# Kernel tuning notes

Measured on AMD Instinct MI355X. Metric: run time of the kernel, lower is better.

Reference implementation:

```python
import jax, jax.numpy as jnp
import numpy as np

N, D, H, E, K = 8192, 1024, 2048, 8, 2
LN_EPS = 1e-5


def setup_inputs() -> dict:
    key = jax.random.key(0)
    ks = jax.random.split(key, 9)
    s_in = 1.0 / np.sqrt(D)
    s_h = 1.0 / np.sqrt(H)
    return {
        "x": jax.random.normal(ks[0], (N, D), jnp.float32),
        "W1": jax.random.uniform(ks[1], (E, D, H), jnp.float32, -s_in, s_in),
        "b1": jax.random.uniform(ks[2], (E, H), jnp.float32, -s_in, s_in),
        "ln_g": jnp.ones((E, H), jnp.float32),
        "ln_b": jnp.zeros((E, H), jnp.float32),
        "W2": jax.random.uniform(ks[3], (E, H, H), jnp.float32, -s_h, s_h),
        "b2": jax.random.uniform(ks[4], (E, H), jnp.float32, -s_h, s_h),
        "Wg": jax.random.uniform(ks[5], (D, E), jnp.float32, -s_in, s_in),
        "bg": jax.random.uniform(ks[6], (E,), jnp.float32, -s_in, s_in),
    }


def _moe(x, W1, b1, ln_g, ln_b, W2, b2, Wg, bg):
    # Gate: softmax over experts, then top-k and renormalize
    gate = jax.nn.softmax(x @ Wg + bg, axis=-1)          # [N, E]
    top_w, top_i = jax.lax.top_k(gate, K)                 # [N, K]
    top_w = top_w / jnp.sum(top_w, axis=-1, keepdims=True)

    # Dense all-expert FFN (faithful to the original: compute every expert)
    h = jnp.einsum('nd,edh->neh', x, W1) + b1[None]       # [N, E, H]
    mu = jnp.mean(h, axis=-1, keepdims=True)
    var = jnp.mean(jnp.square(h - mu), axis=-1, keepdims=True)
    h = (h - mu) * jax.lax.rsqrt(var + LN_EPS) * ln_g[None] + ln_b[None]
    h = jax.nn.gelu(h, approximate=False)                 # torch GELU default = erf
    eo = jnp.einsum('neh,ehk->nek', h, W2) + b2[None]     # [N, E, H]

    # Gather top-k expert outputs and combine
    sel = jnp.take_along_axis(eo, top_i[:, :, None], axis=1)  # [N, K, H]
    return jnp.sum(sel * top_w[:, :, None], axis=1)           # [N, H]


def reference(x, W1, b1, ln_g, ln_b, W2, b2, Wg, bg):
    return _moe(x, W1, b1, ln_g, ln_b, W2, b2, Wg, bg)
```

## Files before the change

### kernel.cpp

```cpp
#include <hip/hip_runtime.h>

#define NTOK 8192
#define DDIM 1024
#define HDIM 2048
#define NEXP 8
#define BM 288
#define NRMAX 29

typedef __attribute__((ext_vector_type(8))) short short8;
typedef __attribute__((ext_vector_type(4))) float f32x4;

static __device__ __forceinline__ unsigned short f2bf(float f){
  unsigned u = __builtin_bit_cast(unsigned, f);
  u += 0x7fffu + ((u >> 16) & 1u);
  return (unsigned short)(u >> 16);
}
static __device__ __forceinline__ float bf2f(unsigned short s){
  unsigned u = ((unsigned)s) << 16;
  return __builtin_bit_cast(float, u);
}

static __device__ __forceinline__ void gload16(const void* g, void* l){
  __builtin_amdgcn_global_load_lds((const __attribute__((address_space(1))) void*)g,
                                   (__attribute__((address_space(3))) void*)l, 16, 0, 0);
}

__global__ __launch_bounds__(256) void transpose_cvt_kernel(const float* __restrict__ src,
    unsigned short* __restrict__ dst, int R, int C){
  int e = blockIdx.z;
  src += (size_t)e * R * C;
  dst += (size_t)e * R * C;
  __shared__ float tile[32][33];
  int c0 = blockIdx.x * 32, r0 = blockIdx.y * 32;
  int t = threadIdx.x;
  {
    int lr = t >> 3, lc = (t & 7) * 4;
    float4 v = *(const float4*)&src[(size_t)(r0 + lr) * C + c0 + lc];
    tile[lr][lc + 0] = v.x; tile[lr][lc + 1] = v.y;
    tile[lr][lc + 2] = v.z; tile[lr][lc + 3] = v.w;
  }
  __syncthreads();
  {
    int lc = t >> 3, lr = (t & 7) * 4;
    ushort4 o;
    o.x = f2bf(tile[lr + 0][lc]);
    o.y = f2bf(tile[lr + 1][lc]);
    o.z = f2bf(tile[lr + 2][lc]);
    o.w = f2bf(tile[lr + 3][lc]);
    *(ushort4*)&dst[(size_t)(c0 + lc) * R + r0 + lr] = o;
  }
}

__global__ __launch_bounds__(256) void gate_kernel(const float* __restrict__ x,
    const float* __restrict__ Wg, const float* __restrict__ bg,
    unsigned short* __restrict__ xbf,
    int* __restrict__ se, float* __restrict__ sw){
  int lane = threadIdx.x & 63;
  int n = blockIdx.x * 4 + (threadIdx.x >> 6);
  const float* xr = x + (size_t)n * DDIM + lane * 16;
  float vv[16];
  #pragma unroll
  for(int i = 0; i < 4; i++){
    float4 v4 = *(const float4*)(xr + i * 4);
    vv[i*4+0] = v4.x; vv[i*4+1] = v4.y; vv[i*4+2] = v4.z; vv[i*4+3] = v4.w;
  }
  {
    uint4 p0, p1;
    unsigned pk[8];
    #pragma unroll
    for(int j = 0; j < 8; j++)
      pk[j] = (unsigned)f2bf(vv[2*j]) | ((unsigned)f2bf(vv[2*j+1]) << 16);
    p0.x = pk[0]; p0.y = pk[1]; p0.z = pk[2]; p0.w = pk[3];
    p1.x = pk[4]; p1.y = pk[5]; p1.z = pk[6]; p1.w = pk[7];
    unsigned short* xw = xbf + (size_t)n * DDIM + lane * 16;
    *(uint4*)xw = p0;
    *(uint4*)(xw + 8) = p1;
  }
  float acc[8] = {0,0,0,0,0,0,0,0};
  #pragma unroll
  for(int j = 0; j < 16; j++){
    const float4* wg = (const float4*)&Wg[(lane * 16 + j) * NEXP];
    float4 a = wg[0], b = wg[1];
    float xv = vv[j];
    acc[0] += xv * a.x; acc[1] += xv * a.y; acc[2] += xv * a.z; acc[3] += xv * a.w;
    acc[4] += xv * b.x; acc[5] += xv * b.y; acc[6] += xv * b.z; acc[7] += xv * b.w;
  }
  #pragma unroll
  for(int e = 0; e < 8; e++){
    #pragma unroll
    for(int o = 32; o; o >>= 1) acc[e] += __shfl_xor(acc[e], o);
  }
  float l[8];
  #pragma unroll
  for(int e = 0; e < 8; e++) l[e] = acc[e] + bg[e];
  int i0 = 0; float l0 = l[0];
  #pragma unroll
  for(int e = 1; e < 8; e++) if(l[e] > l0){ l0 = l[e]; i0 = e; }
  int i1 = -1; float l1 = -3.4e38f;
  #pragma unroll
  for(int e = 0; e < 8; e++) if(e != i0 && l[e] > l1){ l1 = l[e]; i1 = e; }
  float w0 = 1.0f / (1.0f + expf(l1 - l0));
  float w1 = 1.0f - w0;
  if(lane == 0){
    se[2*n] = i0; se[2*n+1] = i1;
    sw[2*n] = w0; sw[2*n+1] = w1;
  }
}

__global__ __launch_bounds__(1024) void build_lists_kernel(const int* __restrict__ se,
    int* __restrict__ toklist, int* __restrict__ sp, int* __restrict__ cnt){
  int e = blockIdx.x;
  int t = threadIdx.x;
  int lane = t & 63, wv = t >> 6;
  __shared__ int wsum[16];
  __shared__ int runbase;
  if(t == 0) runbase = 0;
  __syncthreads();
  for(int base = 0; base < 2 * NTOK; base += 1024){
    int g = base + t;
    bool mine = (se[g] == e);
    unsigned long long m = __ballot(mine);
    int wcnt = __popcll(m);
    int before = __popcll(m & ((1ull << lane) - 1ull));
    if(lane == 0) wsum[wv] = wcnt;
    __syncthreads();
    int wbase = 0, total = 0;
    #pragma unroll
    for(int i = 0; i < 16; i++){
      int s = wsum[i];
      wbase += (i < wv) ? s : 0;
      total += s;
    }
    int pos = runbase + wbase + before;
    if(mine){
      toklist[e * NTOK + pos] = g >> 1;
      sp[g] = pos;
    }
    __syncthreads();
    if(t == 0) runbase += total;
    __syncthreads();
  }
  if(t == 0) cnt[e] = runbase;
}

__global__ void prefix_kernel(const int* __restrict__ cnt, int* __restrict__ base){
  if(threadIdx.x == 0){
    int s = 0;
    for(int e = 0; e < NEXP; e++){ base[e] = s; s += cnt[e]; }
  }
}

#define ADST(buf, i) ((char*)&A_s[buf][0] + (i)*8192 + wbase)
#define BDST(buf, i) ((char*)&B_s[buf][0] + (i)*8192 + wbase)

#define KLOOP_PIPE(NT)                                                                \
  {                                  \
    _Pragma("unroll")                                                                 \
    for(int i = 0; i < 4; i++) gload16(bptr[i], BDST(0, i));                          \
    _Pragma("unroll")                                                                 \
    for(int i = 0; i < 4; i++) gload16(aptr[i], ADST(0, i));                          \
    if(ahalf) gload16(aptr[4], ADST(0, 4));                                           \
    _Pragma("unroll")                                                                 \
    for(int i = 0; i < 4; i++) gload16(bptr[i] + 64, BDST(1, i));                     \
    __builtin_amdgcn_sched_barrier(0);                                                \
    asm volatile("s_waitcnt vmcnt(4)" ::: "memory");                                  \
    __builtin_amdgcn_sched_barrier(0);                                                \
    __builtin_amdgcn_s_barrier();                                                     \
    __builtin_amdgcn_sched_barrier(0);                                                \
  }                                                                                   \
  const int ch0 = ((fg) ^ (fr & 7)) << 3;                                             \
  const int ch1 = ((4 + fg) ^ (fr & 7)) << 3;                                         \
  for(int kt = 0; kt < (NT); ++kt){                                                   \
    const int p = kt & 1;                                                             \
    const unsigned short* Ab = &A_s[p][0];                                            \
    const unsigned short* Bb = &B_s[p][0];                                            \
    short8 bq[4][2];                                                                  \
    _Pragma("unroll")                                                                 \
    for(int q = 0; q < 5; ++q){                                                       \
      const int nmm = (q == 4) ? 1 : 2;                                               \
      short8 af[2][2];                                                                \
      _Pragma("unroll")                                                               \
      for(int mm = 0; mm < 2; ++mm){                                                  \
        if(mm < nmm){                                                                 \
          int row = wr*144 + (q*2 + mm)*16 + fr;                                      \
          af[mm][0] = *(const short8*)&Ab[row*64 + ch0];                              \
          af[mm][1] = *(const short8*)&Ab[row*64 + ch1];                              \
        }                                                                             \
      }                                                                               \
      if(q == 0){                                                                     \
        _Pragma("unroll")                                                             \
        for(int nn = 0; nn < 4; ++nn){                                                \
          int col = wc*64 + nn*16 + fr;                                               \
          bq[nn][0] = *(const short8*)&Bb[col*64 + ch0];                              \
          bq[nn][1] = *(const short8*)&Bb[col*64 + ch1];                              \
        }                                                                             \
      }                                                                               \
      if(q == 0 && kt+1 < (NT)){                                                      \
        gload16(aptr[0] + (kt+1)*64, ADST(p^1, 0));                                   \
        gload16(aptr[1] + (kt+1)*64, ADST(p^1, 1));                                   \
      } else if(q == 1 && kt+1 < (NT)){                                               \
        gload16(aptr[2] + (kt+1)*64, ADST(p^1, 2));                                   \
        gload16(aptr[3] + (kt+1)*64, ADST(p^1, 3));                                   \
      } else if(q == 2){                                                              \
        if(kt+1 < (NT) && ahalf) gload16(aptr[4] + (kt+1)*64, ADST(p^1, 4));          \
        if(kt+2 < (NT)) gload16(bptr[0] + (kt+2)*64, BDST(p, 0));                     \
      } else if(q == 3 && kt+2 < (NT)){                                               \
        gload16(bptr[1] + (kt+2)*64, BDST(p, 1));                                     \
        gload16(bptr[2] + (kt+2)*64, BDST(p, 2));                                     \
      } else if(q == 4 && kt+2 < (NT)){                                               \
        gload16(bptr[3] + (kt+2)*64, BDST(p, 3));                                     \
      }                                                                               \
      __builtin_amdgcn_sched_barrier(0);                                              \
      __builtin_amdgcn_s_barrier();                                                   \
      __builtin_amdgcn_sched_barrier(0);                                              \
      __builtin_amdgcn_s_setprio(1);                                                  \
      _Pragma("unroll")                                                               \
      for(int mm = 0; mm < 2; ++mm){                                                  \
        if(mm < nmm){                                                                 \
          _Pragma("unroll")                                                           \
          for(int nn = 0; nn < 4; ++nn){                                              \
            acc[q*2+mm][nn] = __builtin_amdgcn_mfma_f32_16x16x32_bf16(af[mm][0], bq[nn][0], acc[q*2+mm][nn], 0, 0, 0); \
            acc[q*2+mm][nn] = __builtin_amdgcn_mfma_f32_16x16x32_bf16(af[mm][1], bq[nn][1], acc[q*2+mm][nn], 0, 0, 0); \
          }                                                                           \
        }                                                                             \
      }                                                                               \
      __builtin_amdgcn_s_setprio(0);                                                  \
      __builtin_amdgcn_sched_barrier(0);                                              \
      if(q == 4){                                                                     \
        if(kt < (NT)-2)      { asm volatile("s_waitcnt vmcnt(4)" ::: "memory"); }     \
        else if(kt < (NT)-1) { asm volatile("s_waitcnt vmcnt(0)" ::: "memory"); }     \
      }                                                                               \
      __builtin_amdgcn_s_barrier();                                                   \
      __builtin_amdgcn_sched_barrier(0);                                              \
    }                                                                                 \
  }

__global__ __launch_bounds__(512) void gemm1_kernel(const unsigned short* __restrict__ xbf,
    const unsigned short* __restrict__ W1T, const float* __restrict__ b1,
    const int* __restrict__ cnt, const int* __restrict__ base,
    const int* __restrict__ toklist, unsigned short* __restrict__ hbuf){
  int d = blockIdx.x;
  int e = d & 7;
  int cnt_e = cnt[e];
  int row0 = (d >> 6) * BM;
  if(row0 >= cnt_e) return;
  int col0 = ((d >> 3) & 7) * 256;
  __shared__ __align__(16) unsigned short A_s[2][BM * 64];
  __shared__ __align__(16) unsigned short B_s[2][256 * 64];
  __shared__ int tok_s[BM];
  int t = threadIdx.x;
  if(t < BM){
    int r = row0 + t;
    tok_s[t] = (r < cnt_e) ? toklist[e * NTOK + r] : toklist[e * NTOK + cnt_e - 1];
  }
  __syncthreads();
  int lane = t & 63, w = t >> 6;
  int wr = w >> 2, wc = w & 3;
  int fr = lane & 15, fg = lane >> 4;
  int srow = t >> 3;
  int schunk = ((t & 7) ^ (srow & 7)) * 8;
  bool ahalf = t < 256;
  const unsigned short* W1e = W1T + (size_t)e * HDIM * DDIM;
  const unsigned short* aptr[5];
  const unsigned short* bptr[4];
  #pragma unroll
  for(int i = 0; i < 4; i++)
    aptr[i] = xbf + (size_t)tok_s[i * 64 + srow] * DDIM + schunk;
  {
    int r4 = 256 + (ahalf ? srow : 0);
    aptr[4] = xbf + (size_t)tok_s[r4] * DDIM + schunk;
  }
  #pragma unroll
  for(int i = 0; i < 4; i++)
    bptr[i] = W1e + (size_t)(col0 + i * 64 + srow) * DDIM + schunk;
  unsigned wbase = (unsigned)(w << 10);
  f32x4 acc[9][4] = {};
  KLOOP_PIPE(DDIM / 64)
  int slot0 = base[e] + row0;
  #pragma unroll
  for(int m = 0; m < 9; m++){
    #pragma unroll
    for(int i = 0; i < 4; i++){
      int rr = wr*144 + m*16 + fg*4 + i;
      if(row0 + rr < cnt_e){
        size_t rowoff = (size_t)(slot0 + rr) * HDIM;
        #pragma unroll
        for(int nn = 0; nn < 4; nn++){
          int c = col0 + wc*64 + nn*16 + fr;
          float v = acc[m][nn][i] + b1[e * HDIM + c];
          hbuf[rowoff + c] = f2bf(v);
        }
      }
    }
  }
}

__global__ __launch_bounds__(256) void ln_gelu_kernel(unsigned short* __restrict__ hbuf,
    const float* __restrict__ ln_g, const float* __restrict__ ln_b,
    const int* __restrict__ base){
  int s = blockIdx.x;
  int e = 0;
  #pragma unroll
  for(int i = 1; i < NEXP; i++) if(s >= base[i]) e = i;
  size_t off = (size_t)s * HDIM;
  int t = threadIdx.x;
  uint4 pk = *(const uint4*)&hbuf[off + t * 8];
  float v[8];
  {
    unsigned uu[4] = {pk.x, pk.y, pk.z, pk.w};
    #pragma unroll
    for(int j = 0; j < 4; j++){
      v[2*j]   = bf2f((unsigned short)(uu[j] & 0xffffu));
      v[2*j+1] = bf2f((unsigned short)(uu[j] >> 16));
    }
  }
  float sm = 0.f, ss = 0.f;
  #pragma unroll
  for(int j = 0; j < 8; j++){ sm += v[j]; ss += v[j] * v[j]; }
  #pragma unroll
  for(int o = 32; o; o >>= 1){ sm += __shfl_xor(sm, o); ss += __shfl_xor(ss, o); }
  __shared__ float red[8];
  if((t & 63) == 0){ red[t >> 6] = sm; red[4 + (t >> 6)] = ss; }
  __syncthreads();
  sm = red[0] + red[1] + red[2] + red[3];
  ss = red[4] + red[5] + red[6] + red[7];
  float mean = sm * (1.0f / HDIM);
  float var  = ss * (1.0f / HDIM) - mean * mean;
  float rstd = rsqrtf(var + 1e-5f);
  const float* g  = ln_g + e * HDIM + t * 8;
  const float* bb = ln_b + e * HDIM + t * 8;
  unsigned ou[4];
  #pragma unroll
  for(int j = 0; j < 4; j++){
    float y0 = (v[2*j]   - mean) * rstd * g[2*j]   + bb[2*j];
    float y1 = (v[2*j+1] - mean) * rstd * g[2*j+1] + bb[2*j+1];
    y0 = 0.5f * y0 * (1.0f + erff(y0 * 0.70710678118654752f));
    y1 = 0.5f * y1 * (1.0f + erff(y1 * 0.70710678118654752f));
    ou[j] = (unsigned)f2bf(y0) | ((unsigned)f2bf(y1) << 16);
  }
  uint4 o4; o4.x = ou[0]; o4.y = ou[1]; o4.z = ou[2]; o4.w = ou[3];
  *(uint4*)&hbuf[off + t * 8] = o4;
}

__global__ __launch_bounds__(512) void gemm2_kernel(const unsigned short* __restrict__ hbuf,
    const unsigned short* __restrict__ W2T, const float* __restrict__ b2,
    const int* __restrict__ cnt, const int* __restrict__ base,
    unsigned short* __restrict__ eobuf){
  int d = blockIdx.x;
  int e = d & 7;
  int cnt_e = cnt[e];
  int row0 = (d >> 6) * BM;
  if(row0 >= cnt_e) return;
  int col0 = ((d >> 3) & 7) * 256;
  __shared__ __align__(16) unsigned short A_s[2][BM * 64];
  __shared__ __align__(16) unsigned short B_s[2][256 * 64];
  int t = threadIdx.x;
  int lane = t & 63, w = t >> 6;
  int wr = w >> 2, wc = w & 3;
  int fr = lane & 15, fg = lane >> 4;
  int srow = t >> 3;
  int schunk = ((t & 7) ^ (srow & 7)) * 8;
  bool ahalf = t < 256;
  int ebase = base[e];
  const unsigned short* W2e = W2T + (size_t)e * HDIM * HDIM;
  const unsigned short* aptr[5];
  const unsigned short* bptr[4];
  #pragma unroll
  for(int i = 0; i < 4; i++){
    int r = row0 + i * 64 + srow;
    if(r >= cnt_e) r = cnt_e - 1;
    aptr[i] = hbuf + (size_t)(ebase + r) * HDIM + schunk;
  }
  {
    int r4 = row0 + 256 + (ahalf ? srow : 0);
    if(r4 >= cnt_e) r4 = cnt_e - 1;
    aptr[4] = hbuf + (size_t)(ebase + r4) * HDIM + schunk;
  }
  #pragma unroll
  for(int i = 0; i < 4; i++)
    bptr[i] = W2e + (size_t)(col0 + i * 64 + srow) * HDIM + schunk;
  unsigned wbase = (unsigned)(w << 10);
  f32x4 acc[9][4] = {};
  KLOOP_PIPE(HDIM / 64)
  int slot0 = ebase + row0;
  #pragma unroll
  for(int m = 0; m < 9; m++){
    #pragma unroll
    for(int i = 0; i < 4; i++){
      int rr = wr*144 + m*16 + fg*4 + i;
      if(row0 + rr < cnt_e){
        size_t rowoff = (size_t)(slot0 + rr) * HDIM;
        #pragma unroll
        for(int nn = 0; nn < 4; nn++){
          int c = col0 + wc*64 + nn*16 + fr;
          float v = acc[m][nn][i] + b2[e * HDIM + c];
          eobuf[rowoff + c] = f2bf(v);
        }
      }
    }
  }
}

__global__ __launch_bounds__(256) void combine_kernel(const unsigned short* __restrict__ eobuf,
    const int* __restrict__ base, const int* __restrict__ se, const int* __restrict__ sp,
    const float* __restrict__ sw, float* __restrict__ out){
  int n = blockIdx.x, t = threadIdx.x;
  int e0 = se[2*n], e1 = se[2*n+1];
  int s0 = base[e0] + sp[2*n];
  int s1 = base[e1] + sp[2*n+1];
  float w0 = sw[2*n], w1 = sw[2*n+1];
  uint4 p0 = *(const uint4*)&eobuf[(size_t)s0 * HDIM + t * 8];
  uint4 p1 = *(const uint4*)&eobuf[(size_t)s1 * HDIM + t * 8];
  unsigned a[4] = {p0.x, p0.y, p0.z, p0.w};
  unsigned b[4] = {p1.x, p1.y, p1.z, p1.w};
  float o[8];
  #pragma unroll
  for(int j = 0; j < 4; j++){
    o[2*j]   = w0 * bf2f((unsigned short)(a[j] & 0xffffu)) + w1 * bf2f((unsigned short)(b[j] & 0xffffu));
    o[2*j+1] = w0 * bf2f((unsigned short)(a[j] >> 16))     + w1 * bf2f((unsigned short)(b[j] >> 16));
  }
  float4 o0 = {o[0], o[1], o[2], o[3]};
  float4 o1 = {o[4], o[5], o[6], o[7]};
  float* dst = out + (size_t)n * HDIM + t * 8;
  *(float4*)dst = o0;
  *(float4*)(dst + 4) = o1;
}

extern "C" void kernel_launch(void* const* d_in, const int* in_sizes, int n_in,
                              void* d_out, int out_size, void* d_ws, size_t ws_size,
                              hipStream_t stream){
  (void)in_sizes; (void)n_in; (void)out_size; (void)ws_size;
  const float* x   = (const float*)d_in[0];
  const float* W1  = (const float*)d_in[1];
  const float* b1  = (const float*)d_in[2];
  const float* lng = (const float*)d_in[3];
  const float* lnb = (const float*)d_in[4];
  const float* W2  = (const float*)d_in[5];
  const float* b2  = (const float*)d_in[6];
  const float* Wg  = (const float*)d_in[7];
  const float* bg  = (const float*)d_in[8];
  float* out = (float*)d_out;

  char* ws = (char*)d_ws;
  size_t o = 0;
  unsigned short* W1T   = (unsigned short*)(ws + o); o += (size_t)NEXP * HDIM * DDIM * 2;
  unsigned short* W2T   = (unsigned short*)(ws + o); o += (size_t)NEXP * HDIM * HDIM * 2;
  unsigned short* hbuf  = (unsigned short*)(ws + o); o += (size_t)(NTOK * 2 + 512) * HDIM * 2;
  unsigned short* eobuf = (unsigned short*)(ws + o); o += (size_t)(NTOK * 2 + 512) * HDIM * 2;
  unsigned short* xbf   = (unsigned short*)(ws + o); o += (size_t)NTOK * DDIM * 2;
  int*   cnt     = (int*)(ws + o);   o += 128;
  int*   basep   = (int*)(ws + o);   o += 128;
  int*   toklist = (int*)(ws + o);   o += (size_t)NEXP * NTOK * 4;
  int*   se      = (int*)(ws + o);   o += (size_t)NTOK * 2 * 4;
  int*   sp      = (int*)(ws + o);   o += (size_t)NTOK * 2 * 4;
  float* sw      = (float*)(ws + o); o += (size_t)NTOK * 2 * 4;

  transpose_cvt_kernel<<<dim3(HDIM/32, DDIM/32, NEXP), 256, 0, stream>>>(W1, W1T, DDIM, HDIM);
  transpose_cvt_kernel<<<dim3(HDIM/32, HDIM/32, NEXP), 256, 0, stream>>>(W2, W2T, HDIM, HDIM);
  gate_kernel<<<NTOK/4, 256, 0, stream>>>(x, Wg, bg, xbf, se, sw);
  build_lists_kernel<<<NEXP, 1024, 0, stream>>>(se, toklist, sp, cnt);
  prefix_kernel<<<1, 64, 0, stream>>>(cnt, basep);
  gemm1_kernel<<<8 * 8 * NRMAX, 512, 0, stream>>>(xbf, W1T, b1, cnt, basep, toklist, hbuf);
  ln_gelu_kernel<<<NTOK * 2, 256, 0, stream>>>(hbuf, lng, lnb, basep);
  gemm2_kernel<<<8 * 8 * NRMAX, 512, 0, stream>>>(hbuf, W2T, b2, cnt, basep, eobuf);
  combine_kernel<<<NTOK, 256, 0, stream>>>(eobuf, basep, se, sp, sw, out);
}
```

Before: 428.5 us.

## Pre-permute tokens into contiguous expert-sorted buffer and drop prefix kernel

Adds an xperm kernel that gathers the bf16 token rows into a contiguous expert-sorted buffer. GEMM1 can then load A tiles from contiguous rows instead of indirecting through a token list staged in shared memory. The separate prefix kernel is removed, and each kernel recomputes expert base offsets from the counts. The prefetch load schedule inside the k-loop is also rebalanced across the q phases. The cost is an extra gather pass over x, and GEMM1/GEMM2 tail rows now read past cnt_e into padding instead of being clamped.

```diff
diff --git a/kernel.cpp b/kernel.cpp
--- a/kernel.cpp
+++ b/kernel.cpp
@@ -143,11 +143,23 @@
   if(t == 0) cnt[e] = runbase;
 }
 
-__global__ void prefix_kernel(const int* __restrict__ cnt, int* __restrict__ base){
-  if(threadIdx.x == 0){
-    int s = 0;
-    for(int e = 0; e < NEXP; e++){ base[e] = s; s += cnt[e]; }
-  }
+__global__ __launch_bounds__(128) void xperm_kernel(const unsigned short* __restrict__ xbf,
+    const int* __restrict__ cnt, const int* __restrict__ toklist,
+    unsigned short* __restrict__ xperm){
+  int s = blockIdx.x;
+  int pre = 0, e = 0;
+  #pragma unroll
+  for(int i = 1; i < NEXP; i++){
+    pre += cnt[i-1];
+    if(s >= pre) e = i;
+  }
+  int ebase = 0;
+  #pragma unroll
+  for(int i = 0; i < NEXP; i++) ebase += (i < e) ? cnt[i] : 0;
+  int tok = toklist[e * NTOK + (s - ebase)];
+  const uint4* src = (const uint4*)(xbf + (size_t)tok * DDIM);
+  uint4* dst = (uint4*)(xperm + (size_t)s * DDIM);
+  dst[threadIdx.x] = src[threadIdx.x];
 }
 
 #define ADST(buf, i) ((char*)&A_s[buf][0] + (i)*8192 + wbase)
@@ -198,12 +210,12 @@
       if(q == 0 && kt+1 < (NT)){                                                      \
         gload16(aptr[0] + (kt+1)*64, ADST(p^1, 0));                                   \
         gload16(aptr[1] + (kt+1)*64, ADST(p^1, 1));                                   \
+        gload16(aptr[2] + (kt+1)*64, ADST(p^1, 2));                                   \
       } else if(q == 1 && kt+1 < (NT)){                                               \
-        gload16(aptr[2] + (kt+1)*64, ADST(p^1, 2));                                   \
         gload16(aptr[3] + (kt+1)*64, ADST(p^1, 3));                                   \
-      } else if(q == 2){                                                              \
-        if(kt+1 < (NT) && ahalf) gload16(aptr[4] + (kt+1)*64, ADST(p^1, 4));          \
-        if(kt+2 < (NT)) gload16(bptr[0] + (kt+2)*64, BDST(p, 0));                     \
+        if(ahalf) gload16(aptr[4] + (kt+1)*64, ADST(p^1, 4));                         \
+      } else if(q == 2 && kt+2 < (NT)){                                               \
+        gload16(bptr[0] + (kt+2)*64, BDST(p, 0));                                     \
       } else if(q == 3 && kt+2 < (NT)){                                               \
         gload16(bptr[1] + (kt+2)*64, BDST(p, 1));                                     \
         gload16(bptr[2] + (kt+2)*64, BDST(p, 2));                                     \
@@ -235,25 +247,26 @@
     }                                                                                 \
   }
 
-__global__ __launch_bounds__(512) void gemm1_kernel(const unsigned short* __restrict__ xbf,
+static __device__ __forceinline__ int base_of(const int* __restrict__ cnt, int e){
+  int b = 0;
+  #pragma unroll
+  for(int i = 0; i < NEXP; i++) b += (i < e) ? cnt[i] : 0;
+  return b;
+}
+
+__global__ __launch_bounds__(512) void gemm1_kernel(const unsigned short* __restrict__ xperm,
     const unsigned short* __restrict__ W1T, const float* __restrict__ b1,
-    const int* __restrict__ cnt, const int* __restrict__ base,
-    const int* __restrict__ toklist, unsigned short* __restrict__ hbuf){
+    const int* __restrict__ cnt, unsigned short* __restrict__ hbuf){
   int d = blockIdx.x;
   int e = d & 7;
   int cnt_e = cnt[e];
   int row0 = (d >> 6) * BM;
   if(row0 >= cnt_e) return;
   int col0 = ((d >> 3) & 7) * 256;
+  int ebase = base_of(cnt, e);
   __shared__ __align__(16) unsigned short A_s[2][BM * 64];
   __shared__ __align__(16) unsigned short B_s[2][256 * 64];
-  __shared__ int tok_s[BM];
   int t = threadIdx.x;
-  if(t < BM){
-    int r = row0 + t;
-    tok_s[t] = (r < cnt_e) ? toklist[e * NTOK + r] : toklist[e * NTOK + cnt_e - 1];
-  }
-  __syncthreads();
   int lane = t & 63, w = t >> 6;
   int wr = w >> 2, wc = w & 3;
   int fr = lane & 15, fg = lane >> 4;
@@ -265,18 +278,15 @@
   const unsigned short* bptr[4];
   #pragma unroll
   for(int i = 0; i < 4; i++)
-    aptr[i] = xbf + (size_t)tok_s[i * 64 + srow] * DDIM + schunk;
-  {
-    int r4 = 256 + (ahalf ? srow : 0);
-    aptr[4] = xbf + (size_t)tok_s[r4] * DDIM + schunk;
-  }
+    aptr[i] = xperm + (size_t)(ebase + row0 + i * 64 + srow) * DDIM + schunk;
+  aptr[4] = xperm + (size_t)(ebase + row0 + 256 + (ahalf ? srow : 0)) * DDIM + schunk;
   #pragma unroll
   for(int i = 0; i < 4; i++)
     bptr[i] = W1e + (size_t)(col0 + i * 64 + srow) * DDIM + schunk;
   unsigned wbase = (unsigned)(w << 10);
   f32x4 acc[9][4] = {};
   KLOOP_PIPE(DDIM / 64)
-  int slot0 = base[e] + row0;
+  int slot0 = ebase + row0;
   #pragma unroll
   for(int m = 0; m < 9; m++){
     #pragma unroll
@@ -297,11 +307,14 @@
 
 __global__ __launch_bounds__(256) void ln_gelu_kernel(unsigned short* __restrict__ hbuf,
     const float* __restrict__ ln_g, const float* __restrict__ ln_b,
-    const int* __restrict__ base){
+    const int* __restrict__ cnt){
   int s = blockIdx.x;
-  int e = 0;
-  #pragma unroll
-  for(int i = 1; i < NEXP; i++) if(s >= base[i]) e = i;
+  int pre = 0, e = 0;
+  #pragma unroll
+  for(int i = 1; i < NEXP; i++){
+    pre += cnt[i-1];
+    if(s >= pre) e = i;
+  }
   size_t off = (size_t)s * HDIM;
   int t = threadIdx.x;
   uint4 pk = *(const uint4*)&hbuf[off + t * 8];
@@ -344,14 +357,14 @@
 
 __global__ __launch_bounds__(512) void gemm2_kernel(const unsigned short* __restrict__ hbuf,
     const unsigned short* __restrict__ W2T, const float* __restrict__ b2,
-    const int* __restrict__ cnt, const int* __restrict__ base,
-    unsigned short* __restrict__ eobuf){
+    const int* __restrict__ cnt, unsigned short* __restrict__ eobuf){
   int d = blockIdx.x;
   int e = d & 7;
   int cnt_e = cnt[e];
   int row0 = (d >> 6) * BM;
   if(row0 >= cnt_e) return;
   int col0 = ((d >> 3) & 7) * 256;
+  int ebase = base_of(cnt, e);
   __shared__ __align__(16) unsigned short A_s[2][BM * 64];
   __shared__ __align__(16) unsigned short B_s[2][256 * 64];
   int t = threadIdx.x;
@@ -361,21 +374,13 @@
   int srow = t >> 3;
   int schunk = ((t & 7) ^ (srow & 7)) * 8;
   bool ahalf = t < 256;
-  int ebase = base[e];
   const unsigned short* W2e = W2T + (size_t)e * HDIM * HDIM;
   const unsigned short* aptr[5];
   const unsigned short* bptr[4];
   #pragma unroll
-  for(int i = 0; i < 4; i++){
-    int r = row0 + i * 64 + srow;
-    if(r >= cnt_e) r = cnt_e - 1;
-    aptr[i] = hbuf + (size_t)(ebase + r) * HDIM + schunk;
-  }
-  {
-    int r4 = row0 + 256 + (ahalf ? srow : 0);
-    if(r4 >= cnt_e) r4 = cnt_e - 1;
-    aptr[4] = hbuf + (size_t)(ebase + r4) * HDIM + schunk;
-  }
+  for(int i = 0; i < 4; i++)
+    aptr[i] = hbuf + (size_t)(ebase + row0 + i * 64 + srow) * HDIM + schunk;
+  aptr[4] = hbuf + (size_t)(ebase + row0 + 256 + (ahalf ? srow : 0)) * HDIM + schunk;
   #pragma unroll
   for(int i = 0; i < 4; i++)
     bptr[i] = W2e + (size_t)(col0 + i * 64 + srow) * HDIM + schunk;
@@ -402,12 +407,18 @@
 }
 
 __global__ __launch_bounds__(256) void combine_kernel(const unsigned short* __restrict__ eobuf,
-    const int* __restrict__ base, const int* __restrict__ se, const int* __restrict__ sp,
+    const int* __restrict__ cnt, const int* __restrict__ se, const int* __restrict__ sp,
     const float* __restrict__ sw, float* __restrict__ out){
   int n = blockIdx.x, t = threadIdx.x;
+  int pre[NEXP];
+  {
+    int b = 0;
+    #pragma unroll
+    for(int i = 0; i < NEXP; i++){ pre[i] = b; b += cnt[i]; }
+  }
   int e0 = se[2*n], e1 = se[2*n+1];
-  int s0 = base[e0] + sp[2*n];
-  int s1 = base[e1] + sp[2*n+1];
+  int s0 = pre[e0] + sp[2*n];
+  int s1 = pre[e1] + sp[2*n+1];
   float w0 = sw[2*n], w1 = sw[2*n+1];
   uint4 p0 = *(const uint4*)&eobuf[(size_t)s0 * HDIM + t * 8];
   uint4 p1 = *(const uint4*)&eobuf[(size_t)s1 * HDIM + t * 8];
@@ -448,8 +459,8 @@
   unsigned short* hbuf  = (unsigned short*)(ws + o); o += (size_t)(NTOK * 2 + 512) * HDIM * 2;
   unsigned short* eobuf = (unsigned short*)(ws + o); o += (size_t)(NTOK * 2 + 512) * HDIM * 2;
   unsigned short* xbf   = (unsigned short*)(ws + o); o += (size_t)NTOK * DDIM * 2;
+  unsigned short* xperm = (unsigned short*)(ws + o); o += (size_t)(NTOK * 2 + 512) * DDIM * 2;
   int*   cnt     = (int*)(ws + o);   o += 128;
-  int*   basep   = (int*)(ws + o);   o += 128;
   int*   toklist = (int*)(ws + o);   o += (size_t)NEXP * NTOK * 4;
   int*   se      = (int*)(ws + o);   o += (size_t)NTOK * 2 * 4;
   int*   sp      = (int*)(ws + o);   o += (size_t)NTOK * 2 * 4;
@@ -459,9 +470,9 @@
   transpose_cvt_kernel<<<dim3(HDIM/32, HDIM/32, NEXP), 256, 0, stream>>>(W2, W2T, HDIM, HDIM);
   gate_kernel<<<NTOK/4, 256, 0, stream>>>(x, Wg, bg, xbf, se, sw);
   build_lists_kernel<<<NEXP, 1024, 0, stream>>>(se, toklist, sp, cnt);
-  prefix_kernel<<<1, 64, 0, stream>>>(cnt, basep);
-  gemm1_kernel<<<8 * 8 * NRMAX, 512, 0, stream>>>(xbf, W1T, b1, cnt, basep, toklist, hbuf);
-  ln_gelu_kernel<<<NTOK * 2, 256, 0, stream>>>(hbuf, lng, lnb, basep);
-  gemm2_kernel<<<8 * 8 * NRMAX, 512, 0, stream>>>(hbuf, W2T, b2, cnt, basep, eobuf);
-  combine_kernel<<<NTOK, 256, 0, stream>>>(eobuf, basep, se, sp, sw, out);
-}
+  xperm_kernel<<<NTOK * 2, 128, 0, stream>>>(xbf, cnt, toklist, xperm);
+  gemm1_kernel<<<8 * 8 * NRMAX, 512, 0, stream>>>(xperm, W1T, b1, cnt, hbuf);
+  ln_gelu_kernel<<<NTOK * 2, 256, 0, stream>>>(hbuf, lng, lnb, cnt);
+  gemm2_kernel<<<8 * 8 * NRMAX, 512, 0, stream>>>(hbuf, W2T, b2, cnt, eobuf);
+  combine_kernel<<<NTOK, 256, 0, stream>>>(eobuf, cnt, se, sp, sw, out);
+}
```

Result: slower. 437.2 us (+2.0%).
